# Kernel tuning notes

Measured on AMD Instinct MI355X. Metric: run time of the kernel, lower is better.

The kernel has to match this reference:

```python
import jax, jax.numpy as jnp
import numpy as np

B, WARMUP, HID, FEAT = 256, 128, 2048, 1024  # batch, warmup frames, hidden_units, frame_size**2
T_STEPS = 128


def setup_inputs() -> dict:
    key = jax.random.key(0)
    ks = jax.random.split(key, 7)
    s = 0.02  # small init scale keeps the ReLU recurrence numerically stable over 256 steps
    return {
        "inputs": jax.random.normal(ks[0], (B, WARMUP, FEAT), dtype=jnp.float32),
        "W_ih": jax.random.normal(ks[1], (HID, FEAT), dtype=jnp.float32) * s,
        "b_ih": jax.random.normal(ks[2], (HID,), dtype=jnp.float32) * s,
        "W_hh": jax.random.normal(ks[3], (HID, HID), dtype=jnp.float32) * s,
        "b_hh": jax.random.normal(ks[4], (HID,), dtype=jnp.float32) * s,
        "W_fc": jax.random.normal(ks[5], (FEAT, HID), dtype=jnp.float32) * s,
        "b_fc": jax.random.normal(ks[6], (FEAT,), dtype=jnp.float32) * s,
    }


def reference(inputs, W_ih, b_ih, W_hh, b_hh, W_fc, b_fc):
    # RNNCell with relu nonlinearity: h' = relu(x @ W_ih^T + b_ih + h @ W_hh^T + b_hh)
    def cell(h, x):
        return jax.nn.relu(x @ W_ih.T + b_ih + h @ W_hh.T + b_hh)

    def fc(h):
        return h @ W_fc.T + b_fc

    batch = inputs.shape[0]
    h0 = jnp.zeros((batch, W_hh.shape[0]), dtype=inputs.dtype)

    # warmup: scan over the time axis of inputs
    def warm_step(h, x_t):
        return cell(h, x_t), None

    h, _ = jax.lax.scan(warm_step, h0, jnp.swapaxes(inputs, 0, 1))  # [T,B,F] scan
    pred0 = fc(h)  # first prediction

    def ar_step(carry, _):
        pred, h = carry
        h = cell(h, pred)
        pred = fc(h)
        return (pred, h), pred

    (_, _), preds = jax.lax.scan(ar_step, (pred0, h), None, length=T_STEPS)  # preds: [T_STEPS,B,F]
    out = jnp.concatenate([pred0[None], preds], axis=0)  # [T_STEPS+1, B, F]
    return jnp.swapaxes(out, 0, 1)  # [B, T_STEPS+1, F]
```

## Files before the change

### kernel.cpp

```cpp
#include <hip/hip_runtime.h>
#include <stdint.h>

#define HID   2048
#define FEAT  1024
#define BATCH 256
#define TWARM 128
#define TSTEP 128
#define NOUT  129
#define NBLK  384
#define NTHR  384

typedef short    v8s __attribute__((ext_vector_type(8)));
typedef float    v4f __attribute__((ext_vector_type(4)));
typedef uint32_t v4u __attribute__((ext_vector_type(4)));
typedef int32_t  v4i __attribute__((ext_vector_type(4)));

__device__ v4i llvm_amdgcn_raw_buffer_load_i32x4(v4i srsrc, int voffset, int soffset, int aux) __asm("llvm.amdgcn.raw.buffer.load.v4i32");

__device__ __forceinline__ v4i make_srd(const void* p) {
  union { const void* p; uint32_t w[2]; } c; c.p = p;
  v4i srd;
  srd.x = (int)c.w[0];
  srd.y = (int)c.w[1];
  srd.z = (int)0xFFFFFFFFu;
  srd.w = 0x00020000;
  return srd;
}

__device__ __forceinline__ uint32_t bf16_bits(float f) {
  union { float f; uint32_t u; } c; c.f = f;
  return (c.u + 0x8000u) >> 16;
}

__device__ __forceinline__ v4f mfma16(v8s a, v8s b, v4f c) {
  return __builtin_amdgcn_mfma_f32_16x16x32_bf16(a, b, c, 0, 0, 0);
}

__device__ __forceinline__ v8s a_from_f32(const float* p) {
  v4u x0 = *(const v4u*)p;
  v4u x1 = *(const v4u*)(p + 4);
  uint32_t r0 = __builtin_amdgcn_perm(x0.y + 0x8000u, x0.x + 0x8000u, 0x07060302u);
  uint32_t r1 = __builtin_amdgcn_perm(x0.w + 0x8000u, x0.z + 0x8000u, 0x07060302u);
  uint32_t r2 = __builtin_amdgcn_perm(x1.y + 0x8000u, x1.x + 0x8000u, 0x07060302u);
  uint32_t r3 = __builtin_amdgcn_perm(x1.w + 0x8000u, x1.z + 0x8000u, 0x07060302u);
  union { v4u u; v8s s; } c; c.u = (v4u){r0, r1, r2, r3};
  return c.s;
}

__global__ void pack_b(const float* __restrict__ W, uint32_t* __restrict__ out,
                       int K, int total_chunks) {
  int gid = blockIdx.x * blockDim.x + threadIdx.x;
  if (gid >= total_chunks) return;
  int lane = gid & 63, tile = gid >> 6;
  int k_tiles = K >> 5;
  int n_tile = tile / k_tiles;
  int k_tile = tile - n_tile * k_tiles;
  const float* src = W + (size_t)(n_tile * 16 + (lane & 15)) * K + k_tile * 32 + ((lane >> 4) * 8);
  uint32_t w0 = bf16_bits(src[0]) | (bf16_bits(src[1]) << 16);
  uint32_t w1 = bf16_bits(src[2]) | (bf16_bits(src[3]) << 16);
  uint32_t w2 = bf16_bits(src[4]) | (bf16_bits(src[5]) << 16);
  uint32_t w3 = bf16_bits(src[6]) | (bf16_bits(src[7]) << 16);
  *(v4u*)(out + (size_t)gid * 4) = (v4u){w0, w1, w2, w3};
}

__global__ void pack_bT(const float* __restrict__ Wfc, uint16_t* __restrict__ outp) {
  int gid = blockIdx.x * blockDim.x + threadIdx.x;
  int lane = gid & 63, tile = gid >> 6;
  int h_tile = tile >> 5, f_tile = tile & 31;
  int f0 = f_tile * 32 + (lane >> 4) * 8;
  int h  = h_tile * 16 + (lane & 15);
  uint16_t* dst = outp + (size_t)tile * 512 + lane * 8;
  #pragma unroll
  for (int j = 0; j < 8; ++j)
    dst[j] = (uint16_t)bf16_bits(Wfc[(size_t)(f0 + j) * HID + h]);
}

__global__ void bias_comb_k(const float* __restrict__ Wih, const float* __restrict__ b_ih,
                            const float* __restrict__ b_hh, const float* __restrict__ b_fc,
                            float* __restrict__ b_comb, float* __restrict__ b_warm) {
  int wave = threadIdx.x >> 6, lane = threadIdx.x & 63;
  int n = blockIdx.x * 8 + wave;
  const float* wr = Wih + (size_t)n * FEAT;
  float s = 0.f;
  for (int f = lane; f < FEAT; f += 64) s += wr[f] * b_fc[f];
  for (int off = 32; off; off >>= 1) s += __shfl_down(s, off, 64);
  if (lane == 0) {
    b_comb[n] = s + b_ih[n] + b_hh[n];
    b_warm[n] = b_ih[n] + b_hh[n];
  }
}

__global__ __launch_bounds__(512) void comb_gemm(
    const uint16_t* __restrict__ wih_p, const uint16_t* __restrict__ wfcT_p,
    const float* __restrict__ Whh, uint16_t* __restrict__ comb_p)
{
  __shared__ uint16_t scratch[8][640];
  int wave = threadIdx.x >> 6, lane = threadIdx.x & 63;
  int quad = lane >> 4, l15 = lane & 15;
  int id = blockIdx.x * 8 + wave;
  int n_tile = id >> 6;
  int k_tile = id & 63;
  v4f acc0 = {0.f,0.f,0.f,0.f}, acc1 = {0.f,0.f,0.f,0.f};
  const uint16_t* A  = wih_p  + (size_t)n_tile * 32 * 512 + lane * 8;
  const uint16_t* B0 = wfcT_p + (size_t)(k_tile * 2) * 32 * 512 + lane * 8;
  const uint16_t* B1 = B0 + 32 * 512;
  #pragma unroll 8
  for (int f = 0; f < 32; ++f) {
    v8s a = *(const v8s*)(A + f * 512);
    acc0 = mfma16(a, *(const v8s*)(B0 + f * 512), acc0);
    acc1 = mfma16(a, *(const v8s*)(B1 + f * 512), acc1);
  }
  uint16_t* sc = &scratch[wave][0];
  #pragma unroll
  for (int r = 0; r < 4; ++r) {
    int n = n_tile * 16 + quad * 4 + r;
    int h = k_tile * 32 + l15;
    float v0 = acc0[r] + Whh[(size_t)n * HID + h];
    float v1 = acc1[r] + Whh[(size_t)n * HID + h + 16];
    sc[(quad*4+r)*40 + l15]      = (uint16_t)bf16_bits(v0);
    sc[(quad*4+r)*40 + 16 + l15] = (uint16_t)bf16_bits(v1);
  }
  v4u d = *(v4u*)(sc + l15 * 40 + quad * 8);
  *(v4u*)(comb_p + ((size_t)(n_tile * 64 + k_tile)) * 512 + lane * 8) = d;
}

__global__ __launch_bounds__(NTHR, 3) void rnn_persistent(
    const float* __restrict__ X,
    const uint16_t* __restrict__ whh_p, const uint16_t* __restrict__ wih_p,
    const uint16_t* __restrict__ wfc_p, const uint16_t* __restrict__ comb_p,
    const float* __restrict__ b_comb, const float* __restrict__ b_warm,
    const float* __restrict__ b_fc,
    uint16_t* h0, uint16_t* h1,
    float* __restrict__ out, uint32_t* __restrict__ bar)
{
  __shared__ __align__(16) uint16_t abuf[2][8192];
  __shared__ __align__(16) uint16_t scratch[6][384];
  __shared__ int s_slot, s_nx;

  const int tid  = threadIdx.x;
  const int wave = tid >> 6;
  const int lane = tid & 63;
  const int quad = lane >> 4;
  const int l15  = lane & 15;
  const int m_sub = wave & 1;
  const int ct    = wave >> 1;

  int xcd;
  asm volatile("s_getreg_b32 %0, hwreg(HW_REG_XCC_ID)" : "=s"(xcd));
  xcd &= 7;
  uint32_t* xline = bar + 64 * (1 + xcd);

  if (tid == 0) {
    int slot = (int)__hip_atomic_fetch_add(&xline[0], 1u,
                                           __ATOMIC_RELAXED, __HIP_MEMORY_SCOPE_AGENT);
    uint32_t o = __hip_atomic_fetch_add(&bar[0], 1u,
                                        __ATOMIC_RELAXED, __HIP_MEMORY_SCOPE_AGENT);
    if (o == NBLK - 1)
      __hip_atomic_store(&bar[1], 1u, __ATOMIC_RELAXED, __HIP_MEMORY_SCOPE_AGENT);
    while (__hip_atomic_load(&bar[1], __ATOMIC_RELAXED, __HIP_MEMORY_SCOPE_AGENT) == 0)
      __builtin_amdgcn_s_sleep(2);
    s_slot = slot;
    s_nx = (int)__hip_atomic_load(&xline[0], __ATOMIC_RELAXED, __HIP_MEMORY_SCOPE_AGENT);
  }
  __syncthreads();
  const int slot = s_slot;
  const int Nx   = s_nx;

  const int  sl0   = slot;
  const bool has0  = sl0 < 64;
  const int  g0r   = sl0 * 3 + ct;
  const bool cell0 = has0 && (g0r < 128);
  const bool fc0   = has0 && !cell0;
  const int  sl1   = slot + Nx;
  const int  g1r   = sl1 * 3 + ct;
  const bool has1  = (sl1 < 64) && (g1r >= 128);
  const bool has_cellblk = has0 && (sl0 * 3 < 128);
  const bool has_fcblk   = has1 || (has0 && (sl0 * 3 + 2 >= 128));

  const int gc0 = cell0 ? g0r : 0;
  const int gf0 = fc0   ? (g0r - 128) : 0;
  const int gf1 = has1  ? (g1r - 128) : 0;

  float bias_w = 0.f, bias_a = 0.f, bias_f0 = 0.f, bias_f1 = 0.f;
  if (cell0) { bias_w = b_warm[gc0 * 16 + l15]; bias_a = b_comb[gc0 * 16 + l15]; }
  if (fc0)   { bias_f0 = b_fc[gf0 * 16 + l15]; }
  if (has1)  { bias_f1 = b_fc[gf1 * 16 + l15]; }

  const uint16_t* bw_whh = whh_p + (size_t)gc0 * 64 * 512 + lane * 8;
  const uint16_t* bw_cmb = comb_p + (size_t)gc0 * 64 * 512 + lane * 8;
  const uint16_t* bw_fc0 = wfc_p + (size_t)gf0 * 64 * 512 + lane * 8;
  const uint16_t* bw_fc1 = wfc_p + (size_t)gf1 * 64 * 512 + lane * 8;
  const uint16_t* wx     = wih_p + (size_t)gc0 * 32 * 512 + lane * 8;
  const float*    xrow   = X + (size_t)(xcd * 32 + m_sub * 16 + l15) * TWARM * FEAT + quad * 8;
  const int m_tile = xcd * 2 + m_sub;

  v4i srd_cur = make_srd(h0);
  v4i srd_nxt = make_srd(h1);
  uint16_t* hn = h1;

  v4i p0, p1, p2;
  auto stage_issue = [&](int s) {
    int b0 = ((xcd * 128 + 8 * s) << 10);
    int b1 = b0 + (64 << 10);
    p0 = llvm_amdgcn_raw_buffer_load_i32x4(srd_cur, b0 + tid * 16, 0, 1);
    int i1 = tid + 384;
    p1 = llvm_amdgcn_raw_buffer_load_i32x4(
        srd_cur, (i1 < 512) ? (b0 + i1 * 16) : (b1 + (i1 - 512) * 16), 0, 1);
    if (tid < 256)
      p2 = llvm_amdgcn_raw_buffer_load_i32x4(srd_cur, b1 + (tid + 256) * 16, 0, 1);
  };
  auto stage_write = [&](int bsel) {
    *(v4i*)(&abuf[bsel][0] + tid * 8) = p0;
    *(v4i*)(&abuf[bsel][0] + (tid + 384) * 8) = p1;
    if (tid < 256) *(v4i*)(&abuf[bsel][0] + (tid + 768) * 8) = p2;
  };

  #pragma unroll 1
  for (int t = 0; t <= TWARM + TSTEP; ++t) {
    const bool warm = t < TWARM;
    const bool doh  = t > 0;
    const bool m0 = doh && (cell0 ? (t < TWARM + TSTEP) : (fc0 && t >= TWARM));
    const bool m1 = has1 && (t >= TWARM);
    const bool any_now = doh && ((has_cellblk && t < TWARM + TSTEP) ||
                                 (has_fcblk && t >= TWARM));

    v4f acc0 = {0.f, 0.f, 0.f, 0.f};
    v4f acc1 = {0.f, 0.f, 0.f, 0.f};

    if (any_now) stage_issue(0);

    if (warm && cell0) {
      const float* xr = xrow + (size_t)t * FEAT;
      #pragma unroll 4
      for (int ks = 0; ks < 32; ++ks)
        acc0 = mfma16(a_from_f32(xr + ks * 32), *(const v8s*)(wx + (size_t)ks * 512), acc0);
    }

    if (any_now) {
      stage_write(0);
      __syncthreads();
      const uint16_t* bb0base = cell0 ? (warm ? bw_whh : bw_cmb) : bw_fc0;
      #pragma unroll 1
      for (int s8 = 0; s8 < 8; ++s8) {
        if (s8 < 7) stage_issue(s8 + 1);
        const uint16_t* ab = &abuf[s8 & 1][m_sub * 4096] + lane * 8;
        const uint16_t* bb0 = bb0base + (size_t)(8 * s8) * 512;
        const uint16_t* bb1 = bw_fc1 + (size_t)(8 * s8) * 512;
        if (m0 && m1) {
          #pragma unroll
          for (int kt = 0; kt < 8; ++kt) {
            v8s a = *(const v8s*)(ab + kt * 512);
            acc0 = mfma16(a, *(const v8s*)(bb0 + kt * 512), acc0);
            acc1 = mfma16(a, *(const v8s*)(bb1 + kt * 512), acc1);
          }
        } else if (m0) {
          #pragma unroll
          for (int kt = 0; kt < 8; ++kt)
            acc0 = mfma16(*(const v8s*)(ab + kt * 512), *(const v8s*)(bb0 + kt * 512), acc0);
        } else if (m1) {
          #pragma unroll
          for (int kt = 0; kt < 8; ++kt)
            acc1 = mfma16(*(const v8s*)(ab + kt * 512), *(const v8s*)(bb1 + kt * 512), acc1);
        }
        if (s8 < 7) stage_write((s8 + 1) & 1);
        __syncthreads();
      }
    }

    if (cell0 && t < TWARM + TSTEP) {
      float b = warm ? bias_w : bias_a;
      uint16_t* scw = &scratch[wave][0];
      #pragma unroll
      for (int r = 0; r < 4; ++r) {
        float v = acc0[r] + b; v = v > 0.f ? v : 0.f;
        scw[(quad * 4 + r) * 24 + l15] = (uint16_t)bf16_bits(v);
      }
      if (lane < 32) {
        v4u d = *(const v4u*)(scw + l15 * 24 + (lane >> 4) * 8);
        *(v4u*)((char*)hn + ((m_tile * 64 + (gc0 >> 1)) << 10) + (gc0 & 1) * 512 + lane * 16) = d;
      }
    } else if (fc0 && t >= TWARM) {
      int s = t - TWARM;
      #pragma unroll
      for (int r = 0; r < 4; ++r) {
        int row = xcd * 32 + m_sub * 16 + quad * 4 + r;
        out[((size_t)row * NOUT + s) * FEAT + gf0 * 16 + l15] = acc0[r] + bias_f0;
      }
    }
    if (m1) {
      int s = t - TWARM;
      #pragma unroll
      for (int r = 0; r < 4; ++r) {
        int row = xcd * 32 + m_sub * 16 + quad * 4 + r;
        out[((size_t)row * NOUT + s) * FEAT + gf1 * 16 + l15] = acc1[r] + bias_f1;
      }
    }

    if (t < TWARM + TSTEP) {
      __syncthreads();
      if (tid == 0) {
        uint32_t o = __hip_atomic_fetch_add(&xline[2], 1u,
                                            __ATOMIC_RELAXED, __HIP_MEMORY_SCOPE_AGENT);
        if (o == (uint32_t)((t + 1) * Nx - 1))
          __hip_atomic_store(&xline[3], (uint32_t)(t + 1),
                             __ATOMIC_RELAXED, __HIP_MEMORY_SCOPE_AGENT);
        while (__hip_atomic_load(&xline[3], __ATOMIC_RELAXED,
                                 __HIP_MEMORY_SCOPE_AGENT) < (uint32_t)(t + 1))
          __builtin_amdgcn_s_sleep(2);
      }
      __syncthreads();
      v4i ts = srd_cur; srd_cur = srd_nxt; srd_nxt = ts;
      hn = (hn == h1) ? h0 : h1;
    }
  }
}

extern "C" void kernel_launch(void* const* d_in, const int* in_sizes, int n_in,
                              void* d_out, int out_size, void* d_ws, size_t ws_size,
                              hipStream_t stream) {
  const float* X   = (const float*)d_in[0];
  const float* Wih = (const float*)d_in[1];
  const float* bih = (const float*)d_in[2];
  const float* bhh = (const float*)d_in[4];
  const float* Whh = (const float*)d_in[3];
  const float* Wfc = (const float*)d_in[5];
  const float* bfc = (const float*)d_in[6];
  float* out = (float*)d_out;

  char* ws = (char*)d_ws;
  uint32_t* bar    = (uint32_t*)(ws + 0);
  uint16_t* h0     = (uint16_t*)(ws + 4096);
  uint16_t* h1     = (uint16_t*)(ws + 4096 + 1048576);
  uint16_t* whh_p  = (uint16_t*)(ws + 2101248);
  uint16_t* wih_p  = (uint16_t*)(ws + 10489856);
  uint16_t* wfc_p  = (uint16_t*)(ws + 14684160);
  uint16_t* wfcT_p = (uint16_t*)(ws + 18878464);
  uint16_t* comb_p = (uint16_t*)(ws + 23072768);
  float*    b_comb = (float*)(ws + 31461376);
  float*    b_warm = (float*)(ws + 31469568);

  hipMemsetAsync(bar, 0, 4096, stream);

  pack_b<<<(HID*HID/8)/256, 256, 0, stream>>>(Whh, (uint32_t*)whh_p, HID,  HID*HID/8);
  pack_b<<<(HID*FEAT/8)/256, 256, 0, stream>>>(Wih, (uint32_t*)wih_p, FEAT, HID*FEAT/8);
  pack_b<<<(FEAT*HID/8)/256, 256, 0, stream>>>(Wfc, (uint32_t*)wfc_p, HID,  FEAT*HID/8);
  pack_bT<<<(FEAT*HID/8)/256, 256, 0, stream>>>(Wfc, wfcT_p);
  bias_comb_k<<<256, 512, 0, stream>>>(Wih, bih, bhh, bfc, b_comb, b_warm);
  comb_gemm<<<1024, 512, 0, stream>>>(wih_p, wfcT_p, Whh, comb_p);

  rnn_persistent<<<NBLK, NTHR, 0, stream>>>(X, whh_p, wih_p, wfc_p, comb_p,
                                            b_comb, b_warm, bfc, h0, h1, out, bar);
}
```

Baseline: 8.263 ms.

## Replace LDS-staged hidden state with direct buffer loads and per-wave tile loop

Drops the shared-memory double buffer that staged the hidden state. Each wave now reads its A fragments directly from global memory through buffer loads and computes two 16-row M tiles per weight fragment, so each weight load is reused twice. Work tiles (cell and fc) are spread across waves in a strided loop instead of the fixed slot/ct mapping. Blocks shrink to 4 waves and the barrier counters move to new offsets. This removes the LDS staging and the per-stage __syncthreads, in exchange for redundant global/L2 traffic on the hidden state and possibly worse latency hiding with fewer waves.

```diff
diff --git a/kernel.cpp b/kernel.cpp
--- a/kernel.cpp
+++ b/kernel.cpp
@@ -8,7 +8,7 @@
 #define TSTEP 128
 #define NOUT  129
 #define NBLK  384
-#define NTHR  384
+#define NTHR  256
 
 typedef short    v8s __attribute__((ext_vector_type(8)));
 typedef float    v4f __attribute__((ext_vector_type(4)));
@@ -124,7 +124,7 @@
   *(v4u*)(comb_p + ((size_t)(n_tile * 64 + k_tile)) * 512 + lane * 8) = d;
 }
 
-__global__ __launch_bounds__(NTHR, 3) void rnn_persistent(
+__global__ __launch_bounds__(NTHR, 2) void rnn_persistent(
     const float* __restrict__ X,
     const uint16_t* __restrict__ whh_p, const uint16_t* __restrict__ wih_p,
     const uint16_t* __restrict__ wfc_p, const uint16_t* __restrict__ comb_p,
@@ -133,8 +133,7 @@
     uint16_t* h0, uint16_t* h1,
     float* __restrict__ out, uint32_t* __restrict__ bar)
 {
-  __shared__ __align__(16) uint16_t abuf[2][8192];
-  __shared__ __align__(16) uint16_t scratch[6][384];
+  __shared__ __align__(16) uint16_t scratch[4][384];
   __shared__ int s_slot, s_nx;
 
   const int tid  = threadIdx.x;
@@ -142,8 +141,6 @@
   const int lane = tid & 63;
   const int quad = lane >> 4;
   const int l15  = lane & 15;
-  const int m_sub = wave & 1;
-  const int ct    = wave >> 1;
 
   int xcd;
   asm volatile("s_getreg_b32 %0, hwreg(HW_REG_XCC_ID)" : "=s"(xcd));
@@ -153,11 +150,11 @@
   if (tid == 0) {
     int slot = (int)__hip_atomic_fetch_add(&xline[0], 1u,
                                            __ATOMIC_RELAXED, __HIP_MEMORY_SCOPE_AGENT);
-    uint32_t o = __hip_atomic_fetch_add(&bar[0], 1u,
+    uint32_t o = __hip_atomic_fetch_add(&bar[1016], 1u,
                                         __ATOMIC_RELAXED, __HIP_MEMORY_SCOPE_AGENT);
     if (o == NBLK - 1)
-      __hip_atomic_store(&bar[1], 1u, __ATOMIC_RELAXED, __HIP_MEMORY_SCOPE_AGENT);
-    while (__hip_atomic_load(&bar[1], __ATOMIC_RELAXED, __HIP_MEMORY_SCOPE_AGENT) == 0)
+      __hip_atomic_store(&bar[1017], 1u, __ATOMIC_RELAXED, __HIP_MEMORY_SCOPE_AGENT);
+    while (__hip_atomic_load(&bar[1017], __ATOMIC_RELAXED, __HIP_MEMORY_SCOPE_AGENT) == 0)
       __builtin_amdgcn_s_sleep(2);
     s_slot = slot;
     s_nx = (int)__hip_atomic_load(&xline[0], __ATOMIC_RELAXED, __HIP_MEMORY_SCOPE_AGENT);
@@ -166,133 +163,82 @@
   const int slot = s_slot;
   const int Nx   = s_nx;
 
-  const int  sl0   = slot;
-  const bool has0  = sl0 < 64;
-  const int  g0r   = sl0 * 3 + ct;
-  const bool cell0 = has0 && (g0r < 128);
-  const bool fc0   = has0 && !cell0;
-  const int  sl1   = slot + Nx;
-  const int  g1r   = sl1 * 3 + ct;
-  const bool has1  = (sl1 < 64) && (g1r >= 128);
-  const bool has_cellblk = has0 && (sl0 * 3 < 128);
-  const bool has_fcblk   = has1 || (has0 && (sl0 * 3 + 2 >= 128));
-
-  const int gc0 = cell0 ? g0r : 0;
-  const int gf0 = fc0   ? (g0r - 128) : 0;
-  const int gf1 = has1  ? (g1r - 128) : 0;
-
-  float bias_w = 0.f, bias_a = 0.f, bias_f0 = 0.f, bias_f1 = 0.f;
-  if (cell0) { bias_w = b_warm[gc0 * 16 + l15]; bias_a = b_comb[gc0 * 16 + l15]; }
-  if (fc0)   { bias_f0 = b_fc[gf0 * 16 + l15]; }
-  if (has1)  { bias_f1 = b_fc[gf1 * 16 + l15]; }
-
-  const uint16_t* bw_whh = whh_p + (size_t)gc0 * 64 * 512 + lane * 8;
-  const uint16_t* bw_cmb = comb_p + (size_t)gc0 * 64 * 512 + lane * 8;
-  const uint16_t* bw_fc0 = wfc_p + (size_t)gf0 * 64 * 512 + lane * 8;
-  const uint16_t* bw_fc1 = wfc_p + (size_t)gf1 * 64 * 512 + lane * 8;
-  const uint16_t* wx     = wih_p + (size_t)gc0 * 32 * 512 + lane * 8;
-  const float*    xrow   = X + (size_t)(xcd * 32 + m_sub * 16 + l15) * TWARM * FEAT + quad * 8;
-  const int m_tile = xcd * 2 + m_sub;
-
-  v4i srd_cur = make_srd(h0);
-  v4i srd_nxt = make_srd(h1);
-  uint16_t* hn = h1;
-
-  v4i p0, p1, p2;
-  auto stage_issue = [&](int s) {
-    int b0 = ((xcd * 128 + 8 * s) << 10);
-    int b1 = b0 + (64 << 10);
-    p0 = llvm_amdgcn_raw_buffer_load_i32x4(srd_cur, b0 + tid * 16, 0, 1);
-    int i1 = tid + 384;
-    p1 = llvm_amdgcn_raw_buffer_load_i32x4(
-        srd_cur, (i1 < 512) ? (b0 + i1 * 16) : (b1 + (i1 - 512) * 16), 0, 1);
-    if (tid < 256)
-      p2 = llvm_amdgcn_raw_buffer_load_i32x4(srd_cur, b1 + (tid + 256) * 16, 0, 1);
-  };
-  auto stage_write = [&](int bsel) {
-    *(v4i*)(&abuf[bsel][0] + tid * 8) = p0;
-    *(v4i*)(&abuf[bsel][0] + (tid + 384) * 8) = p1;
-    if (tid < 256) *(v4i*)(&abuf[bsel][0] + (tid + 768) * 8) = p2;
-  };
+  const int a0_off = (((xcd * 2) * 64) << 10) + lane * 16;
+  const int a1_off = a0_off + (64 << 10);
+  const int row0   = xcd * 32;
+
+  v4i srd_cur = make_srd(h0), srd_nxt = make_srd(h1);
+  uint16_t* hw = h1;
 
   #pragma unroll 1
   for (int t = 0; t <= TWARM + TSTEP; ++t) {
     const bool warm = t < TWARM;
-    const bool doh  = t > 0;
-    const bool m0 = doh && (cell0 ? (t < TWARM + TSTEP) : (fc0 && t >= TWARM));
-    const bool m1 = has1 && (t >= TWARM);
-    const bool any_now = doh && ((has_cellblk && t < TWARM + TSTEP) ||
-                                 (has_fcblk && t >= TWARM));
-
-    v4f acc0 = {0.f, 0.f, 0.f, 0.f};
-    v4f acc1 = {0.f, 0.f, 0.f, 0.f};
-
-    if (any_now) stage_issue(0);
-
-    if (warm && cell0) {
-      const float* xr = xrow + (size_t)t * FEAT;
-      #pragma unroll 4
-      for (int ks = 0; ks < 32; ++ks)
-        acc0 = mfma16(a_from_f32(xr + ks * 32), *(const v8s*)(wx + (size_t)ks * 512), acc0);
-    }
-
-    if (any_now) {
-      stage_write(0);
-      __syncthreads();
-      const uint16_t* bb0base = cell0 ? (warm ? bw_whh : bw_cmb) : bw_fc0;
-      #pragma unroll 1
-      for (int s8 = 0; s8 < 8; ++s8) {
-        if (s8 < 7) stage_issue(s8 + 1);
-        const uint16_t* ab = &abuf[s8 & 1][m_sub * 4096] + lane * 8;
-        const uint16_t* bb0 = bb0base + (size_t)(8 * s8) * 512;
-        const uint16_t* bb1 = bw_fc1 + (size_t)(8 * s8) * 512;
-        if (m0 && m1) {
-          #pragma unroll
-          for (int kt = 0; kt < 8; ++kt) {
-            v8s a = *(const v8s*)(ab + kt * 512);
-            acc0 = mfma16(a, *(const v8s*)(bb0 + kt * 512), acc0);
-            acc1 = mfma16(a, *(const v8s*)(bb1 + kt * 512), acc1);
-          }
-        } else if (m0) {
-          #pragma unroll
-          for (int kt = 0; kt < 8; ++kt)
-            acc0 = mfma16(*(const v8s*)(ab + kt * 512), *(const v8s*)(bb0 + kt * 512), acc0);
-        } else if (m1) {
-          #pragma unroll
-          for (int kt = 0; kt < 8; ++kt)
-            acc1 = mfma16(*(const v8s*)(ab + kt * 512), *(const v8s*)(bb1 + kt * 512), acc1);
-        }
-        if (s8 < 7) stage_write((s8 + 1) & 1);
-        __syncthreads();
-      }
-    }
-
-    if (cell0 && t < TWARM + TSTEP) {
-      float b = warm ? bias_w : bias_a;
-      uint16_t* scw = &scratch[wave][0];
-      #pragma unroll
-      for (int r = 0; r < 4; ++r) {
-        float v = acc0[r] + b; v = v > 0.f ? v : 0.f;
-        scw[(quad * 4 + r) * 24 + l15] = (uint16_t)bf16_bits(v);
-      }
-      if (lane < 32) {
-        v4u d = *(const v4u*)(scw + l15 * 24 + (lane >> 4) * 8);
-        *(v4u*)((char*)hn + ((m_tile * 64 + (gc0 >> 1)) << 10) + (gc0 & 1) * 512 + lane * 16) = d;
-      }
-    } else if (fc0 && t >= TWARM) {
-      int s = t - TWARM;
-      #pragma unroll
-      for (int r = 0; r < 4; ++r) {
-        int row = xcd * 32 + m_sub * 16 + quad * 4 + r;
-        out[((size_t)row * NOUT + s) * FEAT + gf0 * 16 + l15] = acc0[r] + bias_f0;
-      }
-    }
-    if (m1) {
-      int s = t - TWARM;
-      #pragma unroll
-      for (int r = 0; r < 4; ++r) {
-        int row = xcd * 32 + m_sub * 16 + quad * 4 + r;
-        out[((size_t)row * NOUT + s) * FEAT + gf1 * 16 + l15] = acc1[r] + bias_f1;
+
+    #pragma unroll 1
+    for (int g = wave * Nx + slot; g < 192; g += 4 * Nx) {
+      const bool is_cell = g < 128;
+      if (is_cell ? (t >= TWARM + TSTEP) : warm) continue;
+
+      v4f acc0 = {0.f, 0.f, 0.f, 0.f};
+      v4f acc1 = {0.f, 0.f, 0.f, 0.f};
+
+      if (warm && is_cell) {
+        const uint16_t* wx = wih_p + (size_t)g * 32 * 512 + lane * 8;
+        const float* xr0 = X + ((size_t)(row0 + l15) * TWARM + t) * FEAT + quad * 8;
+        const float* xr1 = xr0 + (size_t)16 * TWARM * FEAT;
+        #pragma unroll 4
+        for (int ks = 0; ks < 32; ++ks) {
+          v8s wv = *(const v8s*)(wx + (size_t)ks * 512);
+          acc0 = mfma16(a_from_f32(xr0 + ks * 32), wv, acc0);
+          acc1 = mfma16(a_from_f32(xr1 + ks * 32), wv, acc1);
+        }
+      }
+
+      if (t > 0) {
+        const uint16_t* bw = is_cell
+            ? (warm ? whh_p : comb_p) + (size_t)g * 64 * 512 + lane * 8
+            : wfc_p + (size_t)(g - 128) * 64 * 512 + lane * 8;
+        #pragma unroll 8
+        for (int k = 0; k < 64; ++k) {
+          union { v4i i; v8s s; } ca, cb;
+          ca.i = llvm_amdgcn_raw_buffer_load_i32x4(srd_cur, a0_off + k * 1024, 0, 1);
+          cb.i = llvm_amdgcn_raw_buffer_load_i32x4(srd_cur, a1_off + k * 1024, 0, 1);
+          v8s wv = *(const v8s*)(bw + (size_t)k * 512);
+          acc0 = mfma16(ca.s, wv, acc0);
+          acc1 = mfma16(cb.s, wv, acc1);
+        }
+      }
+
+      if (is_cell) {
+        const float b = (warm ? b_warm : b_comb)[g * 16 + l15];
+        uint16_t* scw = &scratch[wave][0];
+        #pragma unroll
+        for (int r = 0; r < 4; ++r) {
+          float v = acc0[r] + b; v = v > 0.f ? v : 0.f;
+          scw[(quad * 4 + r) * 24 + l15] = (uint16_t)bf16_bits(v);
+        }
+        if (lane < 32) {
+          v4u d = *(const v4u*)(scw + l15 * 24 + (lane >> 4) * 8);
+          *(v4u*)((char*)hw + ((((xcd * 2) * 64) + (g >> 1)) << 10) + (g & 1) * 512 + lane * 16) = d;
+        }
+        #pragma unroll
+        for (int r = 0; r < 4; ++r) {
+          float v = acc1[r] + b; v = v > 0.f ? v : 0.f;
+          scw[(quad * 4 + r) * 24 + l15] = (uint16_t)bf16_bits(v);
+        }
+        if (lane < 32) {
+          v4u d = *(const v4u*)(scw + l15 * 24 + (lane >> 4) * 8);
+          *(v4u*)((char*)hw + ((((xcd * 2 + 1) * 64) + (g >> 1)) << 10) + (g & 1) * 512 + lane * 16) = d;
+        }
+      } else {
+        const int s = t - TWARM;
+        const int f0 = (g - 128) * 16 + l15;
+        const float b = b_fc[f0];
+        #pragma unroll
+        for (int r = 0; r < 4; ++r) {
+          out[((size_t)(row0 + quad * 4 + r) * NOUT + s) * FEAT + f0]      = acc0[r] + b;
+          out[((size_t)(row0 + 16 + quad * 4 + r) * NOUT + s) * FEAT + f0] = acc1[r] + b;
+        }
       }
     }
 
@@ -310,7 +256,7 @@
       }
       __syncthreads();
       v4i ts = srd_cur; srd_cur = srd_nxt; srd_nxt = ts;
-      hn = (hn == h1) ? h0 : h1;
+      hw = (hw == h1) ? h0 : h1;
     }
   }
 }
@@ -321,8 +267,8 @@
   const float* X   = (const float*)d_in[0];
   const float* Wih = (const float*)d_in[1];
   const float* bih = (const float*)d_in[2];
+  const float* Whh = (const float*)d_in[3];
   const float* bhh = (const float*)d_in[4];
-  const float* Whh = (const float*)d_in[3];
   const float* Wfc = (const float*)d_in[5];
   const float* bfc = (const float*)d_in[6];
   float* out = (float*)d_out;
```

Measured after the change: 8.079 ms. 1.02x faster.
